# Kernel optimization log

Measured on AMD Instinct MI355X. Metric: run time of the kernel, lower is better.

The kernel has to match this reference:

```python
import jax, jax.numpy as jnp
import numpy as np
from jax import lax

ANG = 9
MIND, MAXD = -4, 4
EPS = 1e-5


def conv(x, w, stride=1, dilation=1, padding=0, groups=1):
    return lax.conv_general_dilated(
        x, w, (stride, stride), [(padding, padding)] * 2,
        rhs_dilation=(dilation, dilation),
        dimension_numbers=('NCHW', 'OIHW', 'NCHW'),
        feature_group_count=groups)


def bn_relu(x, g, b):
    # training-mode BatchNorm2d (biased batch stats) + ReLU, as in torch default forward
    m = x.mean((0, 2, 3), keepdims=True)
    v = ((x - m) ** 2).mean((0, 2, 3), keepdims=True)
    y = (x - m) * lax.rsqrt(v + EPS) * g.reshape(1, -1, 1, 1) + b.reshape(1, -1, 1, 1)
    return jax.nn.relu(y)


def sai2macpi(x, ang):
    # out[:, :, i*ang+u, j*ang+v] = x[:, :, u*h+i, v*w+j]  (pure strided rearrange)
    b, c, hu, wv = x.shape
    h, w = hu // ang, wv // ang
    x = x.reshape(b, c, ang, h, ang, w)
    return x.transpose(0, 1, 3, 2, 5, 4).reshape(b, c, h * ang, w * ang)


def _shift_idx(n, ang, dil, pad):
    # per-view-block gather indices replicating Unfold(k=ang,dil,pad,stride=ang)->Fold
    idx = jnp.arange(n)[:, None] * ang + jnp.arange(ang)[None, :] * dil - pad  # [n, ang]
    valid = (idx >= 0) & (idx < n * ang)
    return jnp.clip(idx, 0, n * ang - 1).reshape(-1), valid.reshape(-1)


def disp_shift(feat, d, ang):
    b, c, hu, wv = feat.shape
    h, w = hu // ang, wv // ang
    if d < 0:
        dil = -d * ang + 1
        pad = ang * (ang - 1) * (-d) // 2
    elif d == 0:
        dil, pad = 1, 0
    else:
        dil = d * ang - 1
        pad = ang * (ang - 1) * d // 2 - ang + 1
    ih, mh = _shift_idx(h, ang, dil, pad)
    iw, mw = _shift_idx(w, ang, dil, pad)
    out = feat[:, :, ih, :][:, :, :, iw]
    mask = (mh[:, None] & mw[None, :]).astype(feat.dtype)
    return out * mask


def setup_inputs() -> dict:
    key = jax.random.key(0)
    ks = jax.random.split(key, 16)
    b, h, w = 2, 96, 96
    hu, wv = h * ANG, w * ANG
    s = 0.1
    inp = {
        'x': jax.random.normal(ks[0], (b, 1, hu, wv), jnp.float32),
        'fw0': jax.random.normal(ks[1], (7, 1, 3, 3), jnp.float32) * s,
        'fg0': jnp.ones((7,), jnp.float32),
        'fb0': jnp.zeros((7,), jnp.float32),
        'fw': jax.random.normal(ks[2], (6, 7, 7, 3, 3), jnp.float32) * s,
        'fg': jnp.ones((6, 7), jnp.float32),
        'fb': jnp.zeros((6, 7), jnp.float32),
        'bc_w': jax.random.normal(ks[3], (144, 7, 9, 9), jnp.float32) * 0.04,
        'agg0_dw': jax.random.normal(ks[4], (144, 1, 3, 3), jnp.float32) * s,
        'agg0_dg': jnp.ones((144,), jnp.float32),
        'agg0_db': jnp.zeros((144,), jnp.float32),
        'agg0_pw': jax.random.normal(ks[5], (180, 144, 1, 1), jnp.float32) * s,
        'agg0_pg': jnp.ones((180,), jnp.float32),
        'agg0_pb': jnp.zeros((180,), jnp.float32),
        'aggm_dw': jax.random.normal(ks[6], (4, 180, 1, 3, 3), jnp.float32) * s,
        'aggm_dg': jnp.ones((4, 180), jnp.float32),
        'aggm_db': jnp.zeros((4, 180), jnp.float32),
        'aggm_pw': jax.random.normal(ks[7], (4, 180, 180, 1, 1), jnp.float32) * s,
        'aggm_pg': jnp.ones((4, 180), jnp.float32),
        'aggm_pb': jnp.zeros((4, 180), jnp.float32),
        'last_dw': jax.random.normal(ks[8], (180, 1, 3, 3), jnp.float32) * s,
        'last_dg': jnp.ones((180,), jnp.float32),
        'last_db': jnp.zeros((180,), jnp.float32),
        'last_pw': jax.random.normal(ks[9], (9, 180, 1, 1), jnp.float32) * s,
    }
    return inp


def reference(x, fw0, fg0, fb0, fw, fg, fb, bc_w,
              agg0_dw, agg0_dg, agg0_db, agg0_pw, agg0_pg, agg0_pb,
              aggm_dw, aggm_dg, aggm_db, aggm_pw, aggm_pg, aggm_pb,
              last_dw, last_dg, last_db, last_pw):
    # SAI -> MacPI rearrange
    f = sai2macpi(x, ANG)
    f = bn_relu(conv(f, fw0, dilation=ANG, padding=ANG), fg0, fb0)
    for i in range(6):
        f = bn_relu(conv(f, fw[i], dilation=ANG, padding=ANG), fg[i], fb[i])
    # per-disparity Unfold/Fold shift -> concat [b, 9*7, hu, wv]
    vol = jnp.concatenate([disp_shift(f, d, ANG) for d in range(MIND, MAXD + 1)], axis=1)
    # BuildCost: grouped conv, kernel=stride=angRes -> [b, 144, h, w]
    cv = conv(vol, bc_w, stride=ANG, groups=9)
    # aggregation: depthwise-separable blocks
    y = bn_relu(conv(cv, agg0_dw, padding=1, groups=144), agg0_dg, agg0_db)
    y = bn_relu(conv(y, agg0_pw), agg0_pg, agg0_pb)
    for i in range(4):
        y = bn_relu(conv(y, aggm_dw[i], padding=1, groups=180), aggm_dg[i], aggm_db[i])
        y = bn_relu(conv(y, aggm_pw[i]), aggm_pg[i], aggm_pb[i])
    y = bn_relu(conv(y, last_dw, padding=1, groups=180), last_dg, last_db)
    cost = conv(y, last_pw)  # [b, 9, h, w]
    score = jax.nn.softmax(cost, axis=1)
    disps = jnp.arange(MIND, MAXD + 1, dtype=score.dtype).reshape(1, -1, 1, 1)
    return jnp.sum(score * disps, axis=1, keepdims=True)  # [b, 1, h, w]
```

## Files before the change

### kernel.cpp

```cpp
#include <hip/hip_runtime.h>

#define ANG 9
#define HH 96
#define BB 2
#define PLANE_F (81*HH*HH)
#define PLANE_A (HH*HH)
#define NBLK_FEAT 1458

__global__ __launch_bounds__(256) void k_bnfinal(const float* __restrict__ psum,
    const float* __restrict__ psq, const float* __restrict__ g, const float* __restrict__ bbias,
    float* __restrict__ sc, float* __restrict__ sh, int NB, float invN) {
  int c = blockIdx.x, tid = threadIdx.x;
  float s = 0.f, q = 0.f;
  for (int k = tid; k < NB; k += 256) { s += psum[c * NB + k]; q += psq[c * NB + k]; }
  __shared__ float ss[256], qq[256];
  ss[tid] = s; qq[tid] = q;
  __syncthreads();
  for (int st = 128; st > 0; st >>= 1) {
    if (tid < st) { ss[tid] += ss[tid + st]; qq[tid] += qq[tid + st]; }
    __syncthreads();
  }
  if (tid == 0) {
    float mean = ss[0] * invN;
    float var = fmaxf(qq[0] * invN - mean * mean, 0.f);
    float scale = g[c] / sqrtf(var + 1e-5f);
    sc[c] = scale; sh[c] = bbias[c] - mean * scale;
  }
}

__global__ __launch_bounds__(256) void k_wprep(const float* __restrict__ bcw,
    const float* __restrict__ a0pw, const float* __restrict__ ampw, const float* __restrict__ lpw,
    float* __restrict__ wt, float* __restrict__ wpt) {
  int k = blockIdx.x * 256 + threadIdx.x;
  if (k < 81648) {
    int o = k & 15; int rest = k >> 4;
    int r81 = rest % 81; int gc = rest / 81;
    int c = gc % 7, g = gc / 7;
    wt[k] = bcw[((g * 16 + o) * 7 + c) * 81 + r81];
    return;
  }
  int t = k - 81648;
  if (t < 25920) {
    int c = t / 180, o = t % 180;
    wpt[t] = a0pw[o * 144 + c];
  } else if (t < 25920 + 129600) {
    int t2 = t - 25920;
    int m = t2 / 32400, r = t2 % 32400;
    int c = r / 180, o = r % 180;
    wpt[t] = ampw[m * 32400 + o * 180 + c];
  } else if (t < 25920 + 129600 + 1620) {
    int t2 = t - 25920 - 129600;
    int c = t2 / 9, o = t2 % 9;
    wpt[t] = lpw[o * 180 + c];
  }
}

__global__ __launch_bounds__(256) void k_featconv0(const float* __restrict__ x,
    const float* __restrict__ w, float* __restrict__ out,
    float* __restrict__ psum, float* __restrict__ psq) {
  int blk = blockIdx.x, tid = threadIdx.x;
  int view = blk / 9, q = blk % 9;
  int b = view / 81, uv = view % 81;
  int u = uv / 9, v = uv % 9;
  int widx = q * 256 + tid;
  int j = widx % HH, i0 = (widx / HH) * 4;
  const float* bx = x + (size_t)b * PLANE_F + (u * HH) * 864 + v * HH;
  int off[6][3]; float m[6][3];
  #pragma unroll
  for (int r6 = 0; r6 < 6; r6++) {
    int ii = i0 + r6 - 1;
    float mi = ((unsigned)ii < 96u) ? 1.f : 0.f;
    int iic = min(max(ii, 0), 95);
    #pragma unroll
    for (int dx = 0; dx < 3; dx++) {
      int jj = j + dx - 1;
      float mj = ((unsigned)jj < 96u) ? 1.f : 0.f;
      int jjc = min(max(jj, 0), 95);
      off[r6][dx] = iic * 864 + jjc;
      m[r6][dx] = mi * mj;
    }
  }
  float win[6][3];
  #pragma unroll
  for (int r6 = 0; r6 < 6; r6++)
    #pragma unroll
    for (int dx = 0; dx < 3; dx++)
      win[r6][dx] = bx[off[r6][dx]] * m[r6][dx];
  float acc[4][7];
  #pragma unroll
  for (int px = 0; px < 4; px++)
    #pragma unroll
    for (int o = 0; o < 7; o++) acc[px][o] = 0.f;
  #pragma unroll
  for (int o = 0; o < 7; o++) {
    const float* wc = w + o * 9;
    #pragma unroll
    for (int ky = 0; ky < 3; ky++)
      #pragma unroll
      for (int kx = 0; kx < 3; kx++) {
        float wv = wc[ky * 3 + kx];
        #pragma unroll
        for (int px = 0; px < 4; px++)
          acc[px][o] = fmaf(win[px + ky][kx], wv, acc[px][o]);
      }
  }
  #pragma unroll
  for (int o = 0; o < 7; o++) {
    float* op = out + ((size_t)(b * 7 + o)) * PLANE_F + uv * PLANE_A + i0 * HH + j;
    #pragma unroll
    for (int px = 0; px < 4; px++) op[px * HH] = acc[px][o];
  }
  float sv[7], qv[7];
  #pragma unroll
  for (int o = 0; o < 7; o++) {
    sv[o] = acc[0][o] + acc[1][o] + acc[2][o] + acc[3][o];
    qv[o] = acc[0][o]*acc[0][o] + acc[1][o]*acc[1][o] + acc[2][o]*acc[2][o] + acc[3][o]*acc[3][o];
  }
  #pragma unroll
  for (int off2 = 32; off2 > 0; off2 >>= 1)
    #pragma unroll
    for (int o = 0; o < 7; o++) { sv[o] += __shfl_down(sv[o], off2); qv[o] += __shfl_down(qv[o], off2); }
  __shared__ float red[4][14];
  int wave = tid >> 6, lane = tid & 63;
  if (lane == 0) {
    #pragma unroll
    for (int o = 0; o < 7; o++) { red[wave][o] = sv[o]; red[wave][7 + o] = qv[o]; }
  }
  __syncthreads();
  if (tid < 14) {
    float t4 = red[0][tid] + red[1][tid] + red[2][tid] + red[3][tid];
    if (tid < 7) psum[tid * NBLK_FEAT + blk] = t4;
    else         psq[(tid - 7) * NBLK_FEAT + blk] = t4;
  }
}

__global__ __launch_bounds__(256) void k_featconv4(const float* __restrict__ in,
    const float* __restrict__ w, const float* __restrict__ sc, const float* __restrict__ sh,
    float* __restrict__ out, float* __restrict__ psum, float* __restrict__ psq) {
  int blk = blockIdx.x, tid = threadIdx.x;
  int view = blk / 9, q = blk % 9;
  int b = view / 81, uv = view % 81;
  int widx = q * 256 + tid;
  int j = widx % HH, i0 = (widx / HH) * 4;
  int off[6][3]; float m[6][3];
  #pragma unroll
  for (int r6 = 0; r6 < 6; r6++) {
    int ii = i0 + r6 - 1;
    float mi = ((unsigned)ii < 96u) ? 1.f : 0.f;
    int iic = min(max(ii, 0), 95);
    #pragma unroll
    for (int dx = 0; dx < 3; dx++) {
      int jj = j + dx - 1;
      float mj = ((unsigned)jj < 96u) ? 1.f : 0.f;
      int jjc = min(max(jj, 0), 95);
      off[r6][dx] = iic * HH + jjc;
      m[r6][dx] = mi * mj;
    }
  }
  float acc[4][7];
  #pragma unroll
  for (int px = 0; px < 4; px++)
    #pragma unroll
    for (int o = 0; o < 7; o++) acc[px][o] = 0.f;
  const float* ipbase = in + ((size_t)(b * 7)) * PLANE_F + uv * PLANE_A;
  float pre[6][3];
  #pragma unroll
  for (int r6 = 0; r6 < 6; r6++)
    #pragma unroll
    for (int dx = 0; dx < 3; dx++)
      pre[r6][dx] = ipbase[off[r6][dx]];
  #pragma unroll 1
  for (int c = 0; c < 7; c++) {
    float s = sc[c], h2 = sh[c];
    float win[6][3];
    #pragma unroll
    for (int r6 = 0; r6 < 6; r6++)
      #pragma unroll
      for (int dx = 0; dx < 3; dx++)
        win[r6][dx] = fmaxf(fmaf(pre[r6][dx], s, h2), 0.f) * m[r6][dx];
    if (c < 6) {
      const float* ipn = ipbase + (size_t)(c + 1) * PLANE_F;
      #pragma unroll
      for (int r6 = 0; r6 < 6; r6++)
        #pragma unroll
        for (int dx = 0; dx < 3; dx++)
          pre[r6][dx] = ipn[off[r6][dx]];
    }
    #pragma unroll
    for (int o = 0; o < 7; o++) {
      const float* wc = w + (o * 7 + c) * 9;
      #pragma unroll
      for (int ky = 0; ky < 3; ky++)
        #pragma unroll
        for (int kx = 0; kx < 3; kx++) {
          float wv = wc[ky * 3 + kx];
          #pragma unroll
          for (int px = 0; px < 4; px++)
            acc[px][o] = fmaf(win[px + ky][kx], wv, acc[px][o]);
        }
    }
  }
  #pragma unroll
  for (int o = 0; o < 7; o++) {
    float* op = out + ((size_t)(b * 7 + o)) * PLANE_F + uv * PLANE_A + i0 * HH + j;
    #pragma unroll
    for (int px = 0; px < 4; px++) op[px * HH] = acc[px][o];
  }
  float sv[7], qv[7];
  #pragma unroll
  for (int o = 0; o < 7; o++) {
    sv[o] = acc[0][o] + acc[1][o] + acc[2][o] + acc[3][o];
    qv[o] = acc[0][o]*acc[0][o] + acc[1][o]*acc[1][o] + acc[2][o]*acc[2][o] + acc[3][o]*acc[3][o];
  }
  #pragma unroll
  for (int off2 = 32; off2 > 0; off2 >>= 1)
    #pragma unroll
    for (int o = 0; o < 7; o++) { sv[o] += __shfl_down(sv[o], off2); qv[o] += __shfl_down(qv[o], off2); }
  __shared__ float red[4][14];
  int wave = tid >> 6, lane = tid & 63;
  if (lane == 0) {
    #pragma unroll
    for (int o = 0; o < 7; o++) { red[wave][o] = sv[o]; red[wave][7 + o] = qv[o]; }
  }
  __syncthreads();
  if (tid < 14) {
    float t4 = red[0][tid] + red[1][tid] + red[2][tid] + red[3][tid];
    if (tid < 7) psum[tid * NBLK_FEAT + blk] = t4;
    else         psq[(tid - 7) * NBLK_FEAT + blk] = t4;
  }
}

__device__ __forceinline__ void bc_load(const float* __restrict__ F, int b, int c, int u,
    int d, int i, int j, float* raw, float* msk) {
  const float* Fc = F + ((size_t)(b * 7 + c)) * PLANE_F + (u * 9) * PLANE_A;
  int ii = i + d * (4 - u);
  float mi = ((unsigned)ii < 96u) ? 1.f : 0.f;
  int iic = min(max(ii, 0), 95);
  const float* Frow = Fc + iic * HH;
  #pragma unroll
  for (int v = 0; v < 9; v++) {
    int jj = j + d * (4 - v);
    float mj = ((unsigned)jj < 96u) ? 1.f : 0.f;
    int jjc = min(max(jj, 0), 95);
    raw[v] = Frow[v * PLANE_A + jjc];
    msk[v] = mi * mj;
  }
}

__global__ __launch_bounds__(256) void k_buildcost(const float* __restrict__ F,
    const float* __restrict__ sc, const float* __restrict__ sh,
    const float* __restrict__ wt, float* __restrict__ cv) {
  int gg = blockIdx.x, b = blockIdx.z, tid = threadIdx.x;
  int g = gg >> 1, half = gg & 1;
  int d = g - 4;
  bool flip = d > 0;
  int p = blockIdx.y * 256 + tid;
  int i = p / HH, j = p % HH;
  float acc[8];
  #pragma unroll
  for (int o = 0; o < 8; o++) acc[o] = 0.f;
  float raw[9], msk[9];
  bc_load(F, b, 0, 0, d, i, j, raw, msk);
  #pragma unroll 1
  for (int cu = 0; cu < 63; cu++) {
    int c = cu / 9, u = cu - c * 9;
    float cr[9], cm[9];
    #pragma unroll
    for (int v = 0; v < 9; v++) { cr[v] = raw[v]; cm[v] = msk[v]; }
    if (cu + 1 < 63) {
      int cn = (cu + 1) / 9, un = (cu + 1) - cn * 9;
      bc_load(F, b, cn, un, d, i, j, raw, msk);
    }
    float s = sc[c], h2 = sh[c];
    int uw = flip ? 8 - u : u;
    const float* wbase = wt + ((size_t)((g * 7 + c) * 81 + uw * 9)) * 16 + half * 8;
    #pragma unroll
    for (int v = 0; v < 9; v++) {
      float a = fmaxf(fmaf(cr[v], s, h2), 0.f) * cm[v];
      int vw = flip ? 8 - v : v;
      const float* wp = wbase + vw * 16;
      #pragma unroll
      for (int o = 0; o < 8; o++) acc[o] = fmaf(wp[o], a, acc[o]);
    }
  }
  size_t cvb = ((size_t)(b * 144 + g * 16 + half * 8)) * PLANE_A + p;
  #pragma unroll
  for (int o = 0; o < 8; o++) cv[cvb + o * PLANE_A] = acc[o];
}

template<bool AFF>
__global__ __launch_bounds__(256) void k_dwconv(const float* __restrict__ in,
    const float* __restrict__ w, const float* __restrict__ isc, const float* __restrict__ ish,
    float* __restrict__ out, float* __restrict__ psum, float* __restrict__ psq, int C) {
  int blk = blockIdx.x, tid = threadIdx.x;
  int q = blk % 9; int rr = blk / 9; int c = rr % C; int b = rr / C;
  int widx = q * 256 + tid;
  int j = widx % HH, i0 = (widx / HH) * 4;
  float s  = AFF ? isc[c] : 1.f;
  float h2 = AFF ? ish[c] : 0.f;
  const float* wc = w + c * 9;
  const float* ip = in + ((size_t)(b * C + c)) * PLANE_A;
  int off[6][3]; float m[6][3];
  #pragma unroll
  for (int r6 = 0; r6 < 6; r6++) {
    int ii = i0 + r6 - 1;
    float mi = ((unsigned)ii < 96u) ? 1.f : 0.f;
    int iic = min(max(ii, 0), 95);
    #pragma unroll
    for (int dx = 0; dx < 3; dx++) {
      int jj = j + dx - 1;
      float mj = ((unsigned)jj < 96u) ? 1.f : 0.f;
      int jjc = min(max(jj, 0), 95);
      off[r6][dx] = iic * HH + jjc;
      m[r6][dx] = mi * mj;
    }
  }
  float win[6][3];
  #pragma unroll
  for (int r6 = 0; r6 < 6; r6++)
    #pragma unroll
    for (int dx = 0; dx < 3; dx++) {
      float vv = ip[off[r6][dx]];
      if (AFF) vv = fmaxf(fmaf(vv, s, h2), 0.f);
      win[r6][dx] = vv * m[r6][dx];
    }
  float acc[4];
  #pragma unroll
  for (int px = 0; px < 4; px++) acc[px] = 0.f;
  #pragma unroll
  for (int ky = 0; ky < 3; ky++)
    #pragma unroll
    for (int kx = 0; kx < 3; kx++) {
      float wv = wc[ky * 3 + kx];
      #pragma unroll
      for (int px = 0; px < 4; px++)
        acc[px] = fmaf(win[px + ky][kx], wv, acc[px]);
    }
  float* op = out + ((size_t)(b * C + c)) * PLANE_A + i0 * HH + j;
  #pragma unroll
  for (int px = 0; px < 4; px++) op[px * HH] = acc[px];
  float sv = acc[0] + acc[1] + acc[2] + acc[3];
  float qv = acc[0]*acc[0] + acc[1]*acc[1] + acc[2]*acc[2] + acc[3]*acc[3];
  #pragma unroll
  for (int off2 = 32; off2 > 0; off2 >>= 1) { sv += __shfl_down(sv, off2); qv += __shfl_down(qv, off2); }
  __shared__ float red[4][2];
  int wave = tid >> 6, lane = tid & 63;
  if (lane == 0) { red[wave][0] = sv; red[wave][1] = qv; }
  __syncthreads();
  if (tid == 0) {
    float S = red[0][0] + red[1][0] + red[2][0] + red[3][0];
    float Q = red[0][1] + red[1][1] + red[2][1] + red[3][1];
    psum[c * 18 + b * 9 + q] = S;
    psq [c * 18 + b * 9 + q] = Q;
  }
}

template<int K>
__global__ __launch_bounds__(256) void k_pwconv(const float* __restrict__ in,
    const float* __restrict__ sc, const float* __restrict__ sh,
    const float* __restrict__ wpt, float* __restrict__ out,
    float* __restrict__ psum, float* __restrict__ psq) {
  int tid = threadIdx.x;
  int posblk = blockIdx.y;
  int p = posblk * 256 + tid;
  int b = p / PLANE_A, pp = p - b * PLANE_A;
  int obase = blockIdx.x * 18;
  float acc[18];
  #pragma unroll
  for (int o = 0; o < 18; o++) acc[o] = 0.f;
  const float* ib = in + (size_t)b * K * PLANE_A + pp;
  float xn[4];
  #pragma unroll
  for (int q2 = 0; q2 < 4; q2++) xn[q2] = ib[(size_t)q2 * PLANE_A];
  #pragma unroll 1
  for (int c0 = 0; c0 < K; c0 += 4) {
    float xv[4];
    #pragma unroll
    for (int q2 = 0; q2 < 4; q2++) xv[q2] = xn[q2];
    if (c0 + 4 < K) {
      #pragma unroll
      for (int q2 = 0; q2 < 4; q2++) xn[q2] = ib[(size_t)(c0 + 4 + q2) * PLANE_A];
    }
    #pragma unroll
    for (int q2 = 0; q2 < 4; q2++) {
      int c = c0 + q2;
      float v = fmaxf(fmaf(xv[q2], sc[c], sh[c]), 0.f);
      const float* wc = wpt + (size_t)c * 180 + obase;
      #pragma unroll
      for (int o = 0; o < 18; o++)
        acc[o] = fmaf(wc[o], v, acc[o]);
    }
  }
  #pragma unroll
  for (int o = 0; o < 18; o++)
    out[((size_t)(b * 180 + obase + o)) * PLANE_A + pp] = acc[o];
  __shared__ float rs[4][18], rq[4][18];
  int wave = tid >> 6, lane = tid & 63;
  #pragma unroll
  for (int o = 0; o < 18; o++) {
    float s = acc[o], q = acc[o] * acc[o];
    #pragma unroll
    for (int off = 32; off > 0; off >>= 1) { s += __shfl_down(s, off); q += __shfl_down(q, off); }
    if (lane == 0) { rs[wave][o] = s; rq[wave][o] = q; }
  }
  __syncthreads();
  if (tid < 18)
    psum[(obase + tid) * 72 + posblk] = rs[0][tid] + rs[1][tid] + rs[2][tid] + rs[3][tid];
  else if (tid < 36) {
    int o = tid - 18;
    psq[(obase + o) * 72 + posblk] = rq[0][o] + rq[1][o] + rq[2][o] + rq[3][o];
  }
}

__global__ __launch_bounds__(256) void k_final(const float* __restrict__ in,
    const float* __restrict__ sc, const float* __restrict__ sh,
    const float* __restrict__ wpt, float* __restrict__ out) {
  int tid = threadIdx.x;
  int t = blockIdx.x * 256 + tid;
  int b = t / PLANE_A, p = t - b * PLANE_A;
  const float* ib = in + (size_t)b * 180 * PLANE_A + p;
  float acc[9];
  #pragma unroll
  for (int o = 0; o < 9; o++) acc[o] = 0.f;
  float xn[4];
  #pragma unroll
  for (int q2 = 0; q2 < 4; q2++) xn[q2] = ib[(size_t)q2 * PLANE_A];
  #pragma unroll 1
  for (int c0 = 0; c0 < 180; c0 += 4) {
    float xv[4];
    #pragma unroll
    for (int q2 = 0; q2 < 4; q2++) xv[q2] = xn[q2];
    if (c0 + 4 < 180) {
      #pragma unroll
      for (int q2 = 0; q2 < 4; q2++) xn[q2] = ib[(size_t)(c0 + 4 + q2) * PLANE_A];
    }
    #pragma unroll
    for (int q2 = 0; q2 < 4; q2++) {
      int c = c0 + q2;
      float v = fmaxf(fmaf(xv[q2], sc[c], sh[c]), 0.f);
      const float* wc = wpt + (size_t)c * 9;
      #pragma unroll
      for (int o = 0; o < 9; o++) acc[o] = fmaf(wc[o], v, acc[o]);
    }
  }
  float m = acc[0];
  #pragma unroll
  for (int o = 1; o < 9; o++) m = fmaxf(m, acc[o]);
  float se = 0.f, num = 0.f;
  #pragma unroll
  for (int o = 0; o < 9; o++) {
    float e = expf(acc[o] - m);
    se += e;
    num += (float)(o - 4) * e;
  }
  out[t] = num / se;
}

extern "C" void kernel_launch(void* const* d_in, const int* in_sizes, int n_in,
                              void* d_out, int out_size, void* d_ws, size_t ws_size,
                              hipStream_t stream) {
  const float* x    = (const float*)d_in[0];
  const float* fw0  = (const float*)d_in[1];
  const float* fg0  = (const float*)d_in[2];
  const float* fb0  = (const float*)d_in[3];
  const float* fw   = (const float*)d_in[4];
  const float* fg   = (const float*)d_in[5];
  const float* fb   = (const float*)d_in[6];
  const float* bcw  = (const float*)d_in[7];
  const float* a0dw = (const float*)d_in[8];
  const float* a0dg = (const float*)d_in[9];
  const float* a0db = (const float*)d_in[10];
  const float* a0pw = (const float*)d_in[11];
  const float* a0pg = (const float*)d_in[12];
  const float* a0pb = (const float*)d_in[13];
  const float* amdw = (const float*)d_in[14];
  const float* amdg = (const float*)d_in[15];
  const float* amdb = (const float*)d_in[16];
  const float* ampw = (const float*)d_in[17];
  const float* ampg = (const float*)d_in[18];
  const float* ampb = (const float*)d_in[19];
  const float* ldw  = (const float*)d_in[20];
  const float* ldg  = (const float*)d_in[21];
  const float* ldb  = (const float*)d_in[22];
  const float* lpw  = (const float*)d_in[23];
  float* outp = (float*)d_out;

  float* FA    = (float*)d_ws;
  float* FB    = FA + (size_t)BB * 7 * PLANE_F;
  float* CV    = FB + (size_t)BB * 7 * PLANE_F;
  float* GA    = CV + (size_t)BB * 144 * PLANE_A;
  float* GB    = GA + (size_t)BB * 180 * PLANE_A;
  float* PSUM  = GB + (size_t)BB * 180 * PLANE_A;
  float* PSQ   = PSUM + 180 * 288;
  float* SC    = PSQ + 180 * 288;
  float* SH    = SC + 180;
  float* WT    = SH + 180;
  float* WPT   = WT + 81648;
  float* WPT_A0 = WPT;
  float* WPT_AM = WPT + 25920;
  float* WPT_L  = WPT + 25920 + 129600;

  const float invNbig = 1.0f / (float)(BB * PLANE_F);
  const float invNsmall = 1.0f / (float)(BB * PLANE_A);

  k_wprep<<<(238788 + 255) / 256, 256, 0, stream>>>(bcw, a0pw, ampw, lpw, WT, WPT);

  k_featconv0<<<NBLK_FEAT, 256, 0, stream>>>(x, fw0, FA, PSUM, PSQ);
  k_bnfinal<<<7, 256, 0, stream>>>(PSUM, PSQ, fg0, fb0, SC, SH, NBLK_FEAT, invNbig);

  float* cur = FA; float* nxt = FB;
  for (int i = 0; i < 6; i++) {
    k_featconv4<<<NBLK_FEAT, 256, 0, stream>>>(cur, fw + i * 441, SC, SH, nxt, PSUM, PSQ);
    k_bnfinal<<<7, 256, 0, stream>>>(PSUM, PSQ, fg + i * 7, fb + i * 7, SC, SH, NBLK_FEAT, invNbig);
    float* tmp = cur; cur = nxt; nxt = tmp;
  }

  k_buildcost<<<dim3(18, 36, 2), 256, 0, stream>>>(cur, SC, SH, WT, CV);

  k_dwconv<false><<<BB * 144 * 9, 256, 0, stream>>>(CV, a0dw, nullptr, nullptr, GA, PSUM, PSQ, 144);
  k_bnfinal<<<144, 256, 0, stream>>>(PSUM, PSQ, a0dg, a0db, SC, SH, 18, invNsmall);
  k_pwconv<144><<<dim3(10, 72), 256, 0, stream>>>(GA, SC, SH, WPT_A0, GB, PSUM, PSQ);
  k_bnfinal<<<180, 256, 0, stream>>>(PSUM, PSQ, a0pg, a0pb, SC, SH, 72, invNsmall);

  for (int m = 0; m < 4; m++) {
    k_dwconv<true><<<BB * 180 * 9, 256, 0, stream>>>(GB, amdw + m * 1620, SC, SH, GA, PSUM, PSQ, 180);
    k_bnfinal<<<180, 256, 0, stream>>>(PSUM, PSQ, amdg + m * 180, amdb + m * 180, SC, SH, 18, invNsmall);
    k_pwconv<180><<<dim3(10, 72), 256, 0, stream>>>(GA, SC, SH, WPT_AM + m * 32400, GB, PSUM, PSQ);
    k_bnfinal<<<180, 256, 0, stream>>>(PSUM, PSQ, ampg + m * 180, ampb + m * 180, SC, SH, 72, invNsmall);
  }

  k_dwconv<true><<<BB * 180 * 9, 256, 0, stream>>>(GB, ldw, SC, SH, GA, PSUM, PSQ, 180);
  k_bnfinal<<<180, 256, 0, stream>>>(PSUM, PSQ, ldg, ldb, SC, SH, 18, invNsmall);

  k_final<<<72, 256, 0, stream>>>(GA, SC, SH, WPT_L, outp);
}
```

Baseline: 795.3 us.

## Stage feature-conv input tiles in shared memory with double buffering

The 3x3 dilated feature convolutions now load a 16-row strip plus halo of each view into LDS once per input channel, applying BN+ReLU and padding masks during the load. Each thread then reads its 6x3 window from LDS instead of issuing 18 masked global loads with per-thread offset math. Blocks become 384 threads covering 16 rows (6 strips per view), and the next channel is double-buffered behind the compute. This cuts redundant global/L2 traffic and BN recomputation, at the cost of LDS use and a barrier per channel.

```diff
diff --git a/kernel.cpp b/kernel.cpp
--- a/kernel.cpp
+++ b/kernel.cpp
@@ -5,7 +5,9 @@
 #define BB 2
 #define PLANE_F (81*HH*HH)
 #define PLANE_A (HH*HH)
-#define NBLK_FEAT 1458
+#define NBLK_FEAT 972
+#define LROW 98
+#define LTILE (18*LROW)
 
 __global__ __launch_bounds__(256) void k_bnfinal(const float* __restrict__ psum,
     const float* __restrict__ psq, const float* __restrict__ g, const float* __restrict__ bbias,
@@ -55,37 +57,56 @@
   }
 }
 
-__global__ __launch_bounds__(256) void k_featconv0(const float* __restrict__ x,
+__device__ __forceinline__ void feat_stats(float (&acc)[4][7], float* __restrict__ psum,
+    float* __restrict__ psq, int blk, int tid) {
+  float sv[7], qv[7];
+  #pragma unroll
+  for (int o = 0; o < 7; o++) {
+    sv[o] = acc[0][o] + acc[1][o] + acc[2][o] + acc[3][o];
+    qv[o] = acc[0][o]*acc[0][o] + acc[1][o]*acc[1][o] + acc[2][o]*acc[2][o] + acc[3][o]*acc[3][o];
+  }
+  #pragma unroll
+  for (int off2 = 32; off2 > 0; off2 >>= 1)
+    #pragma unroll
+    for (int o = 0; o < 7; o++) { sv[o] += __shfl_down(sv[o], off2); qv[o] += __shfl_down(qv[o], off2); }
+  __shared__ float red[6][14];
+  int wave = tid >> 6, lane = tid & 63;
+  if (lane == 0) {
+    #pragma unroll
+    for (int o = 0; o < 7; o++) { red[wave][o] = sv[o]; red[wave][7 + o] = qv[o]; }
+  }
+  __syncthreads();
+  if (tid < 14) {
+    float t6 = red[0][tid] + red[1][tid] + red[2][tid] + red[3][tid] + red[4][tid] + red[5][tid];
+    if (tid < 7) psum[tid * NBLK_FEAT + blk] = t6;
+    else         psq[(tid - 7) * NBLK_FEAT + blk] = t6;
+  }
+}
+
+__global__ __launch_bounds__(384) void k_featconv0(const float* __restrict__ x,
     const float* __restrict__ w, float* __restrict__ out,
     float* __restrict__ psum, float* __restrict__ psq) {
+  __shared__ float buf[LTILE];
   int blk = blockIdx.x, tid = threadIdx.x;
-  int view = blk / 9, q = blk % 9;
-  int b = view / 81, uv = view % 81;
+  int strip = blk % 6; int view = blk / 6;
+  int uv = view % 81, b = view / 81;
   int u = uv / 9, v = uv % 9;
-  int widx = q * 256 + tid;
-  int j = widx % HH, i0 = (widx / HH) * 4;
+  int j = tid % HH, ir = tid / HH;
   const float* bx = x + (size_t)b * PLANE_F + (u * HH) * 864 + v * HH;
-  int off[6][3]; float m[6][3];
-  #pragma unroll
-  for (int r6 = 0; r6 < 6; r6++) {
-    int ii = i0 + r6 - 1;
-    float mi = ((unsigned)ii < 96u) ? 1.f : 0.f;
-    int iic = min(max(ii, 0), 95);
-    #pragma unroll
-    for (int dx = 0; dx < 3; dx++) {
-      int jj = j + dx - 1;
-      float mj = ((unsigned)jj < 96u) ? 1.f : 0.f;
-      int jjc = min(max(jj, 0), 95);
-      off[r6][dx] = iic * 864 + jjc;
-      m[r6][dx] = mi * mj;
-    }
-  }
+  for (int idx = tid; idx < LTILE; idx += 384) {
+    int lr = idx / LROW, lc = idx - lr * LROW;
+    int gr = strip * 16 + lr - 1, gc = lc - 1;
+    float mv = ((unsigned)gr < 96u && (unsigned)gc < 96u) ? 1.f : 0.f;
+    int grc = min(max(gr, 0), 95), gcc = min(max(gc, 0), 95);
+    buf[idx] = bx[grc * 864 + gcc] * mv;
+  }
+  __syncthreads();
   float win[6][3];
   #pragma unroll
   for (int r6 = 0; r6 < 6; r6++)
     #pragma unroll
     for (int dx = 0; dx < 3; dx++)
-      win[r6][dx] = bx[off[r6][dx]] * m[r6][dx];
+      win[r6][dx] = buf[(ir * 4 + r6) * LROW + j + dx];
   float acc[4][7];
   #pragma unroll
   for (int px = 0; px < 4; px++)
@@ -104,87 +125,62 @@
           acc[px][o] = fmaf(win[px + ky][kx], wv, acc[px][o]);
       }
   }
+  int i0 = strip * 16 + ir * 4;
   #pragma unroll
   for (int o = 0; o < 7; o++) {
     float* op = out + ((size_t)(b * 7 + o)) * PLANE_F + uv * PLANE_A + i0 * HH + j;
     #pragma unroll
     for (int px = 0; px < 4; px++) op[px * HH] = acc[px][o];
   }
-  float sv[7], qv[7];
-  #pragma unroll
-  for (int o = 0; o < 7; o++) {
-    sv[o] = acc[0][o] + acc[1][o] + acc[2][o] + acc[3][o];
-    qv[o] = acc[0][o]*acc[0][o] + acc[1][o]*acc[1][o] + acc[2][o]*acc[2][o] + acc[3][o]*acc[3][o];
-  }
-  #pragma unroll
-  for (int off2 = 32; off2 > 0; off2 >>= 1)
-    #pragma unroll
-    for (int o = 0; o < 7; o++) { sv[o] += __shfl_down(sv[o], off2); qv[o] += __shfl_down(qv[o], off2); }
-  __shared__ float red[4][14];
-  int wave = tid >> 6, lane = tid & 63;
-  if (lane == 0) {
-    #pragma unroll
-    for (int o = 0; o < 7; o++) { red[wave][o] = sv[o]; red[wave][7 + o] = qv[o]; }
-  }
-  __syncthreads();
-  if (tid < 14) {
-    float t4 = red[0][tid] + red[1][tid] + red[2][tid] + red[3][tid];
-    if (tid < 7) psum[tid * NBLK_FEAT + blk] = t4;
-    else         psq[(tid - 7) * NBLK_FEAT + blk] = t4;
-  }
-}
-
-__global__ __launch_bounds__(256) void k_featconv4(const float* __restrict__ in,
+  __syncthreads();
+  feat_stats(acc, psum, psq, blk, tid);
+}
+
+__global__ __launch_bounds__(384) void k_featconv4(const float* __restrict__ in,
     const float* __restrict__ w, const float* __restrict__ sc, const float* __restrict__ sh,
     float* __restrict__ out, float* __restrict__ psum, float* __restrict__ psq) {
+  __shared__ float buf[2][LTILE];
   int blk = blockIdx.x, tid = threadIdx.x;
-  int view = blk / 9, q = blk % 9;
-  int b = view / 81, uv = view % 81;
-  int widx = q * 256 + tid;
-  int j = widx % HH, i0 = (widx / HH) * 4;
-  int off[6][3]; float m[6][3];
-  #pragma unroll
-  for (int r6 = 0; r6 < 6; r6++) {
-    int ii = i0 + r6 - 1;
-    float mi = ((unsigned)ii < 96u) ? 1.f : 0.f;
-    int iic = min(max(ii, 0), 95);
-    #pragma unroll
-    for (int dx = 0; dx < 3; dx++) {
-      int jj = j + dx - 1;
-      float mj = ((unsigned)jj < 96u) ? 1.f : 0.f;
-      int jjc = min(max(jj, 0), 95);
-      off[r6][dx] = iic * HH + jjc;
-      m[r6][dx] = mi * mj;
-    }
-  }
+  int strip = blk % 6; int view = blk / 6;
+  int uv = view % 81, b = view / 81;
+  int j = tid % HH, ir = tid / HH;
+  const float* ipbase = in + ((size_t)(b * 7)) * PLANE_F + uv * PLANE_A;
+  {
+    float s = sc[0], h2 = sh[0];
+    const float* ip = ipbase;
+    for (int idx = tid; idx < LTILE; idx += 384) {
+      int lr = idx / LROW, lc = idx - lr * LROW;
+      int gr = strip * 16 + lr - 1, gc = lc - 1;
+      float mv = ((unsigned)gr < 96u && (unsigned)gc < 96u) ? 1.f : 0.f;
+      int grc = min(max(gr, 0), 95), gcc = min(max(gc, 0), 95);
+      buf[0][idx] = fmaxf(fmaf(ip[grc * HH + gcc], s, h2), 0.f) * mv;
+    }
+  }
+  __syncthreads();
   float acc[4][7];
   #pragma unroll
   for (int px = 0; px < 4; px++)
     #pragma unroll
     for (int o = 0; o < 7; o++) acc[px][o] = 0.f;
-  const float* ipbase = in + ((size_t)(b * 7)) * PLANE_F + uv * PLANE_A;
-  float pre[6][3];
-  #pragma unroll
-  for (int r6 = 0; r6 < 6; r6++)
-    #pragma unroll
-    for (int dx = 0; dx < 3; dx++)
-      pre[r6][dx] = ipbase[off[r6][dx]];
   #pragma unroll 1
   for (int c = 0; c < 7; c++) {
-    float s = sc[c], h2 = sh[c];
+    int pb = c & 1;
     float win[6][3];
     #pragma unroll
     for (int r6 = 0; r6 < 6; r6++)
       #pragma unroll
       for (int dx = 0; dx < 3; dx++)
-        win[r6][dx] = fmaxf(fmaf(pre[r6][dx], s, h2), 0.f) * m[r6][dx];
+        win[r6][dx] = buf[pb][(ir * 4 + r6) * LROW + j + dx];
     if (c < 6) {
-      const float* ipn = ipbase + (size_t)(c + 1) * PLANE_F;
-      #pragma unroll
-      for (int r6 = 0; r6 < 6; r6++)
-        #pragma unroll
-        for (int dx = 0; dx < 3; dx++)
-          pre[r6][dx] = ipn[off[r6][dx]];
+      float s = sc[c + 1], h2 = sh[c + 1];
+      const float* ip = ipbase + (size_t)(c + 1) * PLANE_F;
+      for (int idx = tid; idx < LTILE; idx += 384) {
+        int lr = idx / LROW, lc = idx - lr * LROW;
+        int gr = strip * 16 + lr - 1, gc = lc - 1;
+        float mv = ((unsigned)gr < 96u && (unsigned)gc < 96u) ? 1.f : 0.f;
+        int grc = min(max(gr, 0), 95), gcc = min(max(gc, 0), 95);
+        buf[pb ^ 1][idx] = fmaxf(fmaf(ip[grc * HH + gcc], s, h2), 0.f) * mv;
+      }
     }
     #pragma unroll
     for (int o = 0; o < 7; o++) {
@@ -199,35 +195,16 @@
             acc[px][o] = fmaf(win[px + ky][kx], wv, acc[px][o]);
         }
     }
-  }
+    __syncthreads();
+  }
+  int i0 = strip * 16 + ir * 4;
   #pragma unroll
   for (int o = 0; o < 7; o++) {
     float* op = out + ((size_t)(b * 7 + o)) * PLANE_F + uv * PLANE_A + i0 * HH + j;
     #pragma unroll
     for (int px = 0; px < 4; px++) op[px * HH] = acc[px][o];
   }
-  float sv[7], qv[7];
-  #pragma unroll
-  for (int o = 0; o < 7; o++) {
-    sv[o] = acc[0][o] + acc[1][o] + acc[2][o] + acc[3][o];
-    qv[o] = acc[0][o]*acc[0][o] + acc[1][o]*acc[1][o] + acc[2][o]*acc[2][o] + acc[3][o]*acc[3][o];
-  }
-  #pragma unroll
-  for (int off2 = 32; off2 > 0; off2 >>= 1)
-    #pragma unroll
-    for (int o = 0; o < 7; o++) { sv[o] += __shfl_down(sv[o], off2); qv[o] += __shfl_down(qv[o], off2); }
-  __shared__ float red[4][14];
-  int wave = tid >> 6, lane = tid & 63;
-  if (lane == 0) {
-    #pragma unroll
-    for (int o = 0; o < 7; o++) { red[wave][o] = sv[o]; red[wave][7 + o] = qv[o]; }
-  }
-  __syncthreads();
-  if (tid < 14) {
-    float t4 = red[0][tid] + red[1][tid] + red[2][tid] + red[3][tid];
-    if (tid < 7) psum[tid * NBLK_FEAT + blk] = t4;
-    else         psq[(tid - 7) * NBLK_FEAT + blk] = t4;
-  }
+  feat_stats(acc, psum, psq, blk, tid);
 }
 
 __device__ __forceinline__ void bc_load(const float* __restrict__ F, int b, int c, int u,
@@ -505,12 +482,12 @@
 
   k_wprep<<<(238788 + 255) / 256, 256, 0, stream>>>(bcw, a0pw, ampw, lpw, WT, WPT);
 
-  k_featconv0<<<NBLK_FEAT, 256, 0, stream>>>(x, fw0, FA, PSUM, PSQ);
+  k_featconv0<<<NBLK_FEAT, 384, 0, stream>>>(x, fw0, FA, PSUM, PSQ);
   k_bnfinal<<<7, 256, 0, stream>>>(PSUM, PSQ, fg0, fb0, SC, SH, NBLK_FEAT, invNbig);
 
   float* cur = FA; float* nxt = FB;
   for (int i = 0; i < 6; i++) {
-    k_featconv4<<<NBLK_FEAT, 256, 0, stream>>>(cur, fw + i * 441, SC, SH, nxt, PSUM, PSQ);
+    k_featconv4<<<NBLK_FEAT, 384, 0, stream>>>(cur, fw + i * 441, SC, SH, nxt, PSUM, PSQ);
     k_bnfinal<<<7, 256, 0, stream>>>(PSUM, PSQ, fg + i * 7, fb + i * 7, SC, SH, NBLK_FEAT, invNbig);
     float* tmp = cur; cur = nxt; nxt = tmp;
   }
```

Measured after the change: 811.4 us. 2.0% more time.
